# Kernel tuning notes

Hardware: AMD Instinct MI355X
Metric: run time of the kernel (lower is better)

## Reference

```python
import jax, jax.numpy as jnp
import numpy as np
from itertools import combinations

# 2-source PID on the redundancy lattice (Williams-Beer), antichains indexed
# over sources {0,1}; index 2 is the output variable axis.
FULL = (0, 1, 2)
ANTICHAINS = [((0,), (1,)), ((0,),), ((1,),), ((0, 1),)]  # red, unq0, unq1, syn (cumulative I)
MOEBIUS = np.array([[1, 0, 0, 0],
                    [-1, 1, 0, 0],
                    [-1, 0, 1, 0],
                    [1, -1, -1, 1]], dtype=np.float32)
EPS_DEN = 1e-10
EPS_FRAC = 1e-7


def _marginals(p):
    """Powerset marginals of the joint p over axes (0,1,2); trailing axis = neurons."""
    m = {}
    for r in range(1, 4):
        for a in combinations(FULL, r):
            ax = tuple(sorted(set(FULL) - set(a)))
            m[a] = p.sum(ax, keepdims=True) if ax else p
    return m


def _union(m, alpha):
    """Inclusion-exclusion union probability over the sets in antichain alpha."""
    res = 0.0
    for k in range(1, len(alpha) + 1):
        for beta in combinations(alpha, k):
            b_union = tuple(sorted({b for a in beta for b in a}))
            res = res + ((-1) ** (k - 1)) * m[b_union]
    return res


def _isx(m, alpha, p_full):
    """I_cap^sx for one antichain: sum over joint of p * log2 ratio."""
    p_union = jax.lax.stop_gradient(_union(m, alpha))            # no_grad in original
    alpha_t = tuple(tuple(sorted(a + (2,))) for a in alpha)       # append output var
    p_union_t = _union(m, alpha_t)
    frac = p_union_t / (p_union * m[(2,)] + EPS_DEN)
    frac = jnp.where(frac < EPS_FRAC, jnp.asarray(1.0, frac.dtype), frac)
    return (p_full * jnp.log2(frac)).sum((0, 1, 2))               # -> (N,)


def _pid(p):
    m = _marginals(p)
    I_cap = jnp.stack([_isx(m, a, p) for a in ANTICHAINS])        # (4, N)
    Pi = jnp.asarray(MOEBIUS, p.dtype) @ I_cap                    # Moebius transform (4, N)
    p_out = m[(2,)]                                               # (1, 1, out_bins, N)
    H_tot = -(p_out * jnp.log2(p_out + EPS_DEN)).sum(-2)          # (1, 1, N)
    H_res = (H_tot - I_cap[ANTICHAINS.index(((0, 1),))]).reshape(-1)
    return jnp.concatenate([Pi, H_res[None]], axis=0)             # (5, N): red,unq0,unq1,syn,H_res


def setup_inputs() -> dict:
    key = jax.random.key(0)
    # joint histogram over (src1_bins=16, src2_bins=16, out_bins=2, n_neurons=100000)
    p = jax.random.uniform(key, (16, 16, 2, 100000), dtype=jnp.float32)
    p = p / p.sum((0, 1, 2), keepdims=True)  # normalize to a distribution per neuron
    return {"p_all_neurons": p}


def reference(p_all_neurons):
    return _pid(p_all_neurons)
```

## Files before the change

kernel.cpp:

```cpp
#include <hip/hip_runtime.h>

#define LOG2_EPS_CLAMP -23.2534966f

__device__ __forceinline__ float flog2(float x) { return __builtin_amdgcn_logf(x); }

__global__ __launch_bounds__(256) void pid_kernel(const float* __restrict__ p,
                                                  float* __restrict__ out,
                                                  const int N) {
    const int tid = threadIdx.x;
    const int g = tid >> 2;
    const int s = tid & 3;
    const int n = blockIdx.x * 64 + g;
    if (n >= N) return;
    const float* __restrict__ q = p + n;

    float m12p[32];
    #pragma unroll
    for (int t = 0; t < 32; ++t) m12p[t] = 0.f;
    float a0[4], a1[4];

    #pragma unroll
    for (int ii = 0; ii < 4; ++ii) {
        const int i = s * 4 + ii;
        const float* __restrict__ qi = q + (size_t)(i * 32) * (size_t)N;
        float s0 = 0.f, s1 = 0.f;
        #pragma unroll
        for (int j = 0; j < 16; ++j) {
            const float f0 = qi[(size_t)(2 * j) * (size_t)N];
            const float f1 = qi[(size_t)(2 * j + 1) * (size_t)N];
            s0 += f0; s1 += f1;
            m12p[2 * j]     += f0;
            m12p[2 * j + 1] += f1;
        }
        a0[ii] = s0; a1[ii] = s1;
    }

    #pragma unroll
    for (int t = 0; t < 32; ++t) {
        m12p[t] += __shfl_xor(m12p[t], 1, 64);
        m12p[t] += __shfl_xor(m12p[t], 2, 64);
    }

    float P20 = 0.f, P21 = 0.f;
    #pragma unroll
    for (int j = 0; j < 16; ++j) { P20 += m12p[2 * j]; P21 += m12p[2 * j + 1]; }
    const float LP20 = flog2(P20);
    const float LP21 = flog2(P21);

    float I1 = 0.f, I2 = 0.f, I4 = 0.f;
    #pragma unroll
    for (int ii = 0; ii < 4; ++ii) {
        const int i = s * 4 + ii;
        const float a0i = a0[ii], a1i = a1[ii];
        const float m0i = a0i + a1i;
        const float* __restrict__ qi = q + (size_t)(i * 32) * (size_t)N;
        #pragma unroll
        for (int j = 0; j < 16; ++j) {
            const float f0  = qi[(size_t)(2 * j) * (size_t)N];
            const float f1  = qi[(size_t)(2 * j + 1) * (size_t)N];
            const float p01 = f0 + f1;
            const float m1j = m12p[2 * j] + m12p[2 * j + 1];
            const float u1  = m0i + m1j - p01;
            const float Lu1  = flog2(u1);
            const float Lp01 = flog2(p01);
            {
                const float num = a0i + m12p[2 * j] - f0;
                float l1 = flog2(num) - Lu1 - LP20;
                l1 = (l1 < LOG2_EPS_CLAMP) ? 0.f : l1;
                I1 = fmaf(f0, l1, I1);
                float l4 = flog2(f0) - Lp01 - LP20;
                l4 = (l4 < LOG2_EPS_CLAMP) ? 0.f : l4;
                I4 = fmaf(f0, l4, I4);
            }
            {
                const float num = a1i + m12p[2 * j + 1] - f1;
                float l1 = flog2(num) - Lu1 - LP21;
                l1 = (l1 < LOG2_EPS_CLAMP) ? 0.f : l1;
                I1 = fmaf(f1, l1, I1);
                float l4 = flog2(f1) - Lp01 - LP21;
                l4 = (l4 < LOG2_EPS_CLAMP) ? 0.f : l4;
                I4 = fmaf(f1, l4, I4);
            }
        }
        const float L0 = flog2(m0i);
        float la = flog2(a0i) - L0 - LP20;
        la = (la < LOG2_EPS_CLAMP) ? 0.f : la;
        I2 = fmaf(a0i, la, I2);
        float lb = flog2(a1i) - L0 - LP21;
        lb = (lb < LOG2_EPS_CLAMP) ? 0.f : lb;
        I2 = fmaf(a1i, lb, I2);
    }

    I1 += __shfl_xor(I1, 1, 64); I1 += __shfl_xor(I1, 2, 64);
    I2 += __shfl_xor(I2, 1, 64); I2 += __shfl_xor(I2, 2, 64);
    I4 += __shfl_xor(I4, 1, 64); I4 += __shfl_xor(I4, 2, 64);

    float I3 = 0.f;
    #pragma unroll
    for (int j = 0; j < 16; ++j) {
        const float L1 = flog2(m12p[2 * j] + m12p[2 * j + 1]);
        float la = flog2(m12p[2 * j]) - L1 - LP20;
        la = (la < LOG2_EPS_CLAMP) ? 0.f : la;
        I3 = fmaf(m12p[2 * j], la, I3);
        float lb = flog2(m12p[2 * j + 1]) - L1 - LP21;
        lb = (lb < LOG2_EPS_CLAMP) ? 0.f : lb;
        I3 = fmaf(m12p[2 * j + 1], lb, I3);
    }

    const float H = -(P20 * flog2(P20 + 1e-10f) + P21 * flog2(P21 + 1e-10f));

    if (s == 0) {
        out[0 * N + n] = I1;
        out[1 * N + n] = I2 - I1;
        out[2 * N + n] = I3 - I1;
        out[3 * N + n] = I1 - I2 - I3 + I4;
        out[4 * N + n] = H - I4;
    }
}

extern "C" void kernel_launch(void* const* d_in, const int* in_sizes, int n_in,
                              void* d_out, int out_size, void* d_ws, size_t ws_size,
                              hipStream_t stream) {
    const float* p = (const float*)d_in[0];
    float* out = (float*)d_out;
    const int N = in_sizes[0] / 512;
    const int blocks = (N + 63) / 64;
    pid_kernel<<<blocks, 256, 0, stream>>>(p, out, N);
}
```

Before: 285.5 us.

## Remap threads so each wave covers 64 neurons and reduce via shared memory

Changes the thread-to-work mapping so that each wavefront handles 64 consecutive neurons for one slice of source-1 bins, making global loads fully contiguous per wave. Cross-wave reductions of the marginals and partial information sums move from lane shuffles to shared-memory atomics and a shared buffer with block barriers. The final I3/entropy tail is computed only by the first wave. This adds LDS atomic traffic and synchronisation in exchange for better memory coalescing.

```diff
diff --git a/kernel.cpp b/kernel.cpp
--- a/kernel.cpp
+++ b/kernel.cpp
@@ -7,109 +7,125 @@
 __global__ __launch_bounds__(256) void pid_kernel(const float* __restrict__ p,
                                                   float* __restrict__ out,
                                                   const int N) {
+    __shared__ float m12buf[32][64];
+    __shared__ float ibuf[3][4][64];
+
     const int tid = threadIdx.x;
-    const int g = tid >> 2;
-    const int s = tid & 3;
-    const int n = blockIdx.x * 64 + g;
-    if (n >= N) return;
+    const int g   = tid & 63;
+    const int s   = tid >> 6;
+    const int n   = blockIdx.x * 64 + g;
+    const bool active = (n < N);
+
+    #pragma unroll
+    for (int t = 0; t < 8; ++t) ((float*)m12buf)[t * 256 + tid] = 0.f;
+    __syncthreads();
+
     const float* __restrict__ q = p + n;
 
-    float m12p[32];
+    float a0[4], a1[4];
+    float part[32];
     #pragma unroll
-    for (int t = 0; t < 32; ++t) m12p[t] = 0.f;
-    float a0[4], a1[4];
+    for (int t = 0; t < 32; ++t) part[t] = 0.f;
 
+    if (active) {
+        #pragma unroll
+        for (int ii = 0; ii < 4; ++ii) {
+            const int i = s * 4 + ii;
+            const float* __restrict__ qi = q + (size_t)(i * 32) * (size_t)N;
+            float s0 = 0.f, s1 = 0.f;
+            #pragma unroll
+            for (int j = 0; j < 16; ++j) {
+                const float f0 = qi[(size_t)(2 * j) * (size_t)N];
+                const float f1 = qi[(size_t)(2 * j + 1) * (size_t)N];
+                s0 += f0; s1 += f1;
+                part[2 * j]     += f0;
+                part[2 * j + 1] += f1;
+            }
+            a0[ii] = s0; a1[ii] = s1;
+        }
+        #pragma unroll
+        for (int t = 0; t < 32; ++t) atomicAdd(&m12buf[t][g], part[t]);
+    }
+    __syncthreads();
+
+    float m12[32];
     #pragma unroll
-    for (int ii = 0; ii < 4; ++ii) {
-        const int i = s * 4 + ii;
-        const float* __restrict__ qi = q + (size_t)(i * 32) * (size_t)N;
-        float s0 = 0.f, s1 = 0.f;
-        #pragma unroll
-        for (int j = 0; j < 16; ++j) {
-            const float f0 = qi[(size_t)(2 * j) * (size_t)N];
-            const float f1 = qi[(size_t)(2 * j + 1) * (size_t)N];
-            s0 += f0; s1 += f1;
-            m12p[2 * j]     += f0;
-            m12p[2 * j + 1] += f1;
-        }
-        a0[ii] = s0; a1[ii] = s1;
-    }
-
-    #pragma unroll
-    for (int t = 0; t < 32; ++t) {
-        m12p[t] += __shfl_xor(m12p[t], 1, 64);
-        m12p[t] += __shfl_xor(m12p[t], 2, 64);
-    }
+    for (int t = 0; t < 32; ++t) m12[t] = m12buf[t][g];
 
     float P20 = 0.f, P21 = 0.f;
     #pragma unroll
-    for (int j = 0; j < 16; ++j) { P20 += m12p[2 * j]; P21 += m12p[2 * j + 1]; }
+    for (int j = 0; j < 16; ++j) { P20 += m12[2 * j]; P21 += m12[2 * j + 1]; }
     const float LP20 = flog2(P20);
     const float LP21 = flog2(P21);
 
     float I1 = 0.f, I2 = 0.f, I4 = 0.f;
-    #pragma unroll
-    for (int ii = 0; ii < 4; ++ii) {
-        const int i = s * 4 + ii;
-        const float a0i = a0[ii], a1i = a1[ii];
-        const float m0i = a0i + a1i;
-        const float* __restrict__ qi = q + (size_t)(i * 32) * (size_t)N;
+    if (active) {
+        #pragma unroll
+        for (int ii = 0; ii < 4; ++ii) {
+            const int i = s * 4 + ii;
+            const float a0i = a0[ii], a1i = a1[ii];
+            const float m0i = a0i + a1i;
+            const float* __restrict__ qi = q + (size_t)(i * 32) * (size_t)N;
+            #pragma unroll
+            for (int j = 0; j < 16; ++j) {
+                const float f0  = qi[(size_t)(2 * j) * (size_t)N];
+                const float f1  = qi[(size_t)(2 * j + 1) * (size_t)N];
+                const float p01 = f0 + f1;
+                const float m1j = m12[2 * j] + m12[2 * j + 1];
+                const float u1  = m0i + m1j - p01;
+                const float Lu1  = flog2(u1);
+                const float Lp01 = flog2(p01);
+                {
+                    const float num = a0i + m12[2 * j] - f0;
+                    float l1 = flog2(num) - Lu1 - LP20;
+                    l1 = (l1 < LOG2_EPS_CLAMP) ? 0.f : l1;
+                    I1 = fmaf(f0, l1, I1);
+                    float l4 = flog2(f0) - Lp01 - LP20;
+                    l4 = (l4 < LOG2_EPS_CLAMP) ? 0.f : l4;
+                    I4 = fmaf(f0, l4, I4);
+                }
+                {
+                    const float num = a1i + m12[2 * j + 1] - f1;
+                    float l1 = flog2(num) - Lu1 - LP21;
+                    l1 = (l1 < LOG2_EPS_CLAMP) ? 0.f : l1;
+                    I1 = fmaf(f1, l1, I1);
+                    float l4 = flog2(f1) - Lp01 - LP21;
+                    l4 = (l4 < LOG2_EPS_CLAMP) ? 0.f : l4;
+                    I4 = fmaf(f1, l4, I4);
+                }
+            }
+            const float L0 = flog2(m0i);
+            float la = flog2(a0i) - L0 - LP20;
+            la = (la < LOG2_EPS_CLAMP) ? 0.f : la;
+            I2 = fmaf(a0i, la, I2);
+            float lb = flog2(a1i) - L0 - LP21;
+            lb = (lb < LOG2_EPS_CLAMP) ? 0.f : lb;
+            I2 = fmaf(a1i, lb, I2);
+        }
+    }
+    ibuf[0][s][g] = I1;
+    ibuf[1][s][g] = I2;
+    ibuf[2][s][g] = I4;
+    __syncthreads();
+
+    if (s == 0 && active) {
+        I1 = ibuf[0][0][g] + ibuf[0][1][g] + ibuf[0][2][g] + ibuf[0][3][g];
+        I2 = ibuf[1][0][g] + ibuf[1][1][g] + ibuf[1][2][g] + ibuf[1][3][g];
+        I4 = ibuf[2][0][g] + ibuf[2][1][g] + ibuf[2][2][g] + ibuf[2][3][g];
+
+        float I3 = 0.f;
         #pragma unroll
         for (int j = 0; j < 16; ++j) {
-            const float f0  = qi[(size_t)(2 * j) * (size_t)N];
-            const float f1  = qi[(size_t)(2 * j + 1) * (size_t)N];
-            const float p01 = f0 + f1;
-            const float m1j = m12p[2 * j] + m12p[2 * j + 1];
-            const float u1  = m0i + m1j - p01;
-            const float Lu1  = flog2(u1);
-            const float Lp01 = flog2(p01);
-            {
-                const float num = a0i + m12p[2 * j] - f0;
-                float l1 = flog2(num) - Lu1 - LP20;
-                l1 = (l1 < LOG2_EPS_CLAMP) ? 0.f : l1;
-                I1 = fmaf(f0, l1, I1);
-                float l4 = flog2(f0) - Lp01 - LP20;
-                l4 = (l4 < LOG2_EPS_CLAMP) ? 0.f : l4;
-                I4 = fmaf(f0, l4, I4);
-            }
-            {
-                const float num = a1i + m12p[2 * j + 1] - f1;
-                float l1 = flog2(num) - Lu1 - LP21;
-                l1 = (l1 < LOG2_EPS_CLAMP) ? 0.f : l1;
-                I1 = fmaf(f1, l1, I1);
-                float l4 = flog2(f1) - Lp01 - LP21;
-                l4 = (l4 < LOG2_EPS_CLAMP) ? 0.f : l4;
-                I4 = fmaf(f1, l4, I4);
-            }
+            const float L1 = flog2(m12[2 * j] + m12[2 * j + 1]);
+            float la = flog2(m12[2 * j]) - L1 - LP20;
+            la = (la < LOG2_EPS_CLAMP) ? 0.f : la;
+            I3 = fmaf(m12[2 * j], la, I3);
+            float lb = flog2(m12[2 * j + 1]) - L1 - LP21;
+            lb = (lb < LOG2_EPS_CLAMP) ? 0.f : lb;
+            I3 = fmaf(m12[2 * j + 1], lb, I3);
         }
-        const float L0 = flog2(m0i);
-        float la = flog2(a0i) - L0 - LP20;
-        la = (la < LOG2_EPS_CLAMP) ? 0.f : la;
-        I2 = fmaf(a0i, la, I2);
-        float lb = flog2(a1i) - L0 - LP21;
-        lb = (lb < LOG2_EPS_CLAMP) ? 0.f : lb;
-        I2 = fmaf(a1i, lb, I2);
-    }
+        const float H = -(P20 * flog2(P20 + 1e-10f) + P21 * flog2(P21 + 1e-10f));
 
-    I1 += __shfl_xor(I1, 1, 64); I1 += __shfl_xor(I1, 2, 64);
-    I2 += __shfl_xor(I2, 1, 64); I2 += __shfl_xor(I2, 2, 64);
-    I4 += __shfl_xor(I4, 1, 64); I4 += __shfl_xor(I4, 2, 64);
-
-    float I3 = 0.f;
-    #pragma unroll
-    for (int j = 0; j < 16; ++j) {
-        const float L1 = flog2(m12p[2 * j] + m12p[2 * j + 1]);
-        float la = flog2(m12p[2 * j]) - L1 - LP20;
-        la = (la < LOG2_EPS_CLAMP) ? 0.f : la;
-        I3 = fmaf(m12p[2 * j], la, I3);
-        float lb = flog2(m12p[2 * j + 1]) - L1 - LP21;
-        lb = (lb < LOG2_EPS_CLAMP) ? 0.f : lb;
-        I3 = fmaf(m12p[2 * j + 1], lb, I3);
-    }
-
-    const float H = -(P20 * flog2(P20 + 1e-10f) + P21 * flog2(P21 + 1e-10f));
-
-    if (s == 0) {
         out[0 * N + n] = I1;
         out[1 * N + n] = I2 - I1;
         out[2 * N + n] = I3 - I1;
```

Measured after the change: 340.2 us. 1.19x slower.
